# Kernel tuning notes

Hardware: AMD Instinct MI355X
Metric: run time of the kernel (lower is better)

## Reference

```python
import jax, jax.numpy as jnp
import numpy as np

B, S, E, H, L = 2, 2048, 1024, 16, 64


def setup_inputs() -> dict:
    key = jax.random.key(0)
    ks = jax.random.split(key, 9)
    x = jax.random.normal(ks[0], (B, S, E), dtype=jnp.float32)
    # causal mask: 1 where attention allowed, 0 where blocked (mask==0 -> -inf)
    mask = jnp.tril(jnp.ones((1, S, S), dtype=jnp.int32))
    std = 0.02
    # per-head Linear weights stacked over heads; torch Linear stores W as [out, in]
    Wq = jax.random.normal(ks[1], (H, L, E), dtype=jnp.float32) * std
    Wk = jax.random.normal(ks[2], (H, L, E), dtype=jnp.float32) * std
    Wv = jax.random.normal(ks[3], (H, L, E), dtype=jnp.float32) * std
    bq = jax.random.normal(ks[4], (H, L), dtype=jnp.float32) * std
    bk = jax.random.normal(ks[5], (H, L), dtype=jnp.float32) * std
    bv = jax.random.normal(ks[6], (H, L), dtype=jnp.float32) * std
    Wo = jax.random.normal(ks[7], (E, H * L), dtype=jnp.float32) * std
    bo = jax.random.normal(ks[8], (E,), dtype=jnp.float32) * std
    return {"x": x, "mask": mask, "Wq": Wq, "bq": bq, "Wk": Wk, "bk": bk,
            "Wv": Wv, "bv": bv, "Wo": Wo, "bo": bo}


def reference(x, mask, Wq, bq, Wk, bk, Wv, bv, Wo, bo):
    # Q/K/V for all heads at once: [B, H, S, L]
    Q = jnp.einsum('bse,hle->bhsl', x, Wq) + bq[None, :, None, :]
    K = jnp.einsum('bse,hle->bhsl', x, Wk) + bk[None, :, None, :]
    V = jnp.einsum('bse,hle->bhsl', x, Wv) + bv[None, :, None, :]
    scale = jnp.sqrt(jnp.asarray(L, dtype=Q.dtype))
    scores = jnp.einsum('bhsl,bhtl->bhst', Q, K) / scale  # [B,H,S,S]
    scores = jnp.where(mask[:, None, :, :] == 0, -jnp.inf, scores)
    P = jax.nn.softmax(scores, axis=-1)
    O = jnp.einsum('bhst,bhtl->bhsl', P, V)  # [B,H,S,L]
    # concat heads along last dim (head order matches torch concat)
    z = jnp.transpose(O, (0, 2, 1, 3)).reshape(O.shape[0], O.shape[2], -1)
    return jnp.einsum('bsk,ek->bse', z, Wo) + bo
```

## Files before the change

kernel.cpp:

```cpp
#include <hip/hip_runtime.h>
#include <math.h>

typedef unsigned short US;
typedef __attribute__((ext_vector_type(8))) __bf16 bf16x8;
typedef __attribute__((ext_vector_type(4))) float f32x4;
typedef __attribute__((ext_vector_type(4))) unsigned short us4;

#define MFMA16(a, b, c) __builtin_amdgcn_mfma_f32_16x16x32_bf16(a, b, c, 0, 0, 0)

__device__ __forceinline__ US f2bf(float f) {
  union { float f; unsigned u; } v; v.f = f;
  unsigned r = v.u + 0x7fffu + ((v.u >> 16) & 1u);
  return (US)(r >> 16);
}
__device__ __forceinline__ float bf2f(US u) {
  union { unsigned u; float f; } v; v.u = ((unsigned)u) << 16; return v.f;
}

__device__ __forceinline__ void gload16(const void* g, void* l) {
  __builtin_amdgcn_global_load_lds(
      (const __attribute__((address_space(1))) unsigned int*)g,
      (__attribute__((address_space(3))) unsigned int*)l, 16, 0, 0);
}

__global__ __launch_bounds__(256) void convert_k(
    const float* __restrict__ x, const float* __restrict__ Wq,
    const float* __restrict__ Wk, const float* __restrict__ Wv,
    const float* __restrict__ Wo,
    US* __restrict__ xb, US* __restrict__ wqkv, US* __restrict__ wob) {
  long i = (long)blockIdx.x * blockDim.x + threadIdx.x;
  long e4 = i * 4;
  if (e4 >= 8388608L) return;
  const float* src; US* dst;
  if (e4 < 4194304L) { src = x + e4; dst = xb + e4; }
  else if (e4 < 7340032L) {
    long off = e4 - 4194304L;
    dst = wqkv + off;
    src = (off < 1048576L) ? Wq + off
        : (off < 2097152L ? Wk + (off - 1048576L) : Wv + (off - 2097152L));
  } else {
    long off = e4 - 7340032L;
    src = Wo + off; dst = wob + off;
  }
  float4 v = *(const float4*)src;
  us4 o; o.x = f2bf(v.x); o.y = f2bf(v.y); o.z = f2bf(v.z); o.w = f2bf(v.w);
  *(us4*)dst = o;
}

template <int MODE>
__global__ __launch_bounds__(256) void gemm128(
    const US* __restrict__ A, const US* __restrict__ BT,
    int K, int lda, int ldb, int N,
    const float* __restrict__ b0, const float* __restrict__ b1,
    const float* __restrict__ b2,
    US* __restrict__ oQ, US* __restrict__ oK, US* __restrict__ oV,
    float* __restrict__ oF) {
  __shared__ __align__(16) US As[2][128 * 32];
  __shared__ __align__(16) US Bs[2][128 * 32];
  const int tid = threadIdx.x, lane = tid & 63;
  const int w = tid >> 6, wr = w >> 1, wc = w & 1;
  const int m0 = blockIdx.x * 128, n0 = blockIdx.y * 128;
  f32x4 acc[4][4] = {};
  const int r0 = tid >> 2, c0 = (tid & 3) * 8;

  for (int kt = 0; kt < K; kt += 64) {
#pragma unroll
    for (int h = 0; h < 2; ++h) {
      gload16(A + (size_t)(m0 + r0) * lda + kt + h * 32 + c0, As[h] + tid * 8);
      gload16(A + (size_t)(m0 + r0 + 64) * lda + kt + h * 32 + c0,
              As[h] + (tid + 256) * 8);
      gload16(BT + (size_t)(n0 + r0) * ldb + kt + h * 32 + c0, Bs[h] + tid * 8);
      gload16(BT + (size_t)(n0 + r0 + 64) * ldb + kt + h * 32 + c0,
              Bs[h] + (tid + 256) * 8);
    }
    __syncthreads();
#pragma unroll
    for (int h = 0; h < 2; ++h) {
      bf16x8 af[4], bfm[4];
#pragma unroll
      for (int i = 0; i < 4; ++i)
        af[i] = *(const bf16x8*)(As[h] + (wr * 64 + i * 16 + (lane & 15)) * 32 +
                                 (lane >> 4) * 8);
#pragma unroll
      for (int j = 0; j < 4; ++j)
        bfm[j] = *(const bf16x8*)(Bs[h] + (wc * 64 + j * 16 + (lane & 15)) * 32 +
                                  (lane >> 4) * 8);
#pragma unroll
      for (int i = 0; i < 4; ++i)
#pragma unroll
        for (int j = 0; j < 4; ++j)
          acc[i][j] = MFMA16(af[i], bfm[j], acc[i][j]);
    }
    __syncthreads();
  }

#pragma unroll
  for (int i = 0; i < 4; ++i) {
#pragma unroll
    for (int j = 0; j < 4; ++j) {
#pragma unroll
      for (int r = 0; r < 4; ++r) {
        int m = m0 + wr * 64 + i * 16 + (lane >> 4) * 4 + r;
        int n = n0 + wc * 64 + j * 16 + (lane & 15);
        float v = acc[i][j][r];
        if (MODE == 0) {
          int bb = m >> 11, s = m & 2047;
          int sec = n >> 10, idx = n & 1023;
          int h = idx >> 6, l = idx & 63;
          size_t bhsl = (((size_t)bb * 16 + h) * 2048 + s) * 64 + l;
          if (sec == 0)      oQ[bhsl] = f2bf((v + b0[idx]) * 0.18033688f);
          else if (sec == 1) oK[bhsl] = f2bf(v + b1[idx]);
          else oV[(((size_t)bb * 16 + h) * 64 + l) * 2048 + s] = f2bf(v + b2[idx]);
        } else {
          oF[(size_t)m * N + n] = v + b0[n];
        }
      }
    }
  }
}

__global__ __launch_bounds__(256) void attn_k(
    const US* __restrict__ Qb, const US* __restrict__ Kb,
    const US* __restrict__ Vtb, US* __restrict__ opart,
    float2* __restrict__ mlpart) {
  __shared__ __align__(16) US Ks[64 * 64];
  __shared__ __align__(16) US Vs[64 * 64];
  __shared__ __align__(16) US Ps[4][16 * 72];
  const int tid = threadIdx.x, lane = tid & 63, w = tid >> 6;
  const int slot = blockIdx.x >> 6;
  const int qt = 31 - slot;
  const int bh = (blockIdx.x & 63) >> 1;
  const int half = blockIdx.x & 1;
  const int h0 = (qt + 2) >> 1;
  const int kstart = half ? h0 : 0;
  const int kend = half ? (qt + 1) : h0;
  const size_t pslot = (size_t)(bh * 32 + qt) * 2 + half;

  if (kstart >= kend) {
    US* op = opart + pslot * 4096;
    us4 z; z.x = 0; z.y = 0; z.z = 0; z.w = 0;
#pragma unroll
    for (int j = 0; j < 4; ++j) *(us4*)(op + tid * 16 + j * 4) = z;
    if ((lane >> 4) == 0)
      mlpart[pslot * 64 + w * 16 + lane] = make_float2(-INFINITY, 0.f);
    return;
  }

  const US* Qp = Qb + ((size_t)bh * 2048 + qt * 64) * 64;
  const char* Kbase = (const char*)(Kb + (size_t)bh * 2048 * 64);
  const char* Vbase = (const char*)(Vtb + (size_t)bh * 64 * 2048);

  const int row0 = tid >> 3, col16 = (tid & 7) * 16;
  const int row1 = row0 + 32;
  const int soff0 = (row0 * 128 + col16) ^ ((row0 & 7) << 4);
  const int soff1 = soff0 + 32 * 128;

  bf16x8 aq[2];
  {
    int qrow = w * 16 + (lane & 15);
#pragma unroll
    for (int kk = 0; kk < 2; ++kk)
      aq[kk] = *(const bf16x8*)(Qp + qrow * 64 + kk * 32 + (lane >> 4) * 8);
  }
  f32x4 o[4] = {};
  float m = -INFINITY, l = 0.f;

  int4 rk0, rk1, rv0, rv1;
#define LOADT(KT)                                                              \
  do {                                                                         \
    rk0 = *(const int4*)(Kbase + ((size_t)((KT)*64 + row0)) * 128 + col16);    \
    rk1 = *(const int4*)(Kbase + ((size_t)((KT)*64 + row1)) * 128 + col16);    \
    rv0 = *(const int4*)(Vbase + (size_t)row0 * 4096 + (KT)*128 + col16);      \
    rv1 = *(const int4*)(Vbase + (size_t)row1 * 4096 + (KT)*128 + col16);      \
  } while (0)
#define WRITET()                                                               \
  do {                                                                         \
    *(int4*)((char*)Ks + soff0) = rk0;                                         \
    *(int4*)((char*)Ks + soff1) = rk1;                                         \
    *(int4*)((char*)Vs + soff0) = rv0;                                         \
    *(int4*)((char*)Vs + soff1) = rv1;                                         \
  } while (0)

  LOADT(kstart);
  WRITET();
  __syncthreads();

  for (int kt = kstart; kt < kend; ++kt) {
    if (kt + 1 < kend) LOADT(kt + 1);

    f32x4 sc[4];
    __builtin_amdgcn_s_setprio(1);
#pragma unroll
    for (int nt = 0; nt < 4; ++nt) {
      f32x4 s = {0.f, 0.f, 0.f, 0.f};
#pragma unroll
      for (int kk = 0; kk < 2; ++kk) {
        int rr = nt * 16 + (lane & 15);
        int off = rr * 128 + kk * 64 + (lane >> 4) * 16;
        off ^= (rr & 7) << 4;
        bf16x8 bkf = *(const bf16x8*)((const char*)Ks + off);
        s = MFMA16(bkf, aq[kk], s);
      }
      sc[nt] = s;
    }
    __builtin_amdgcn_s_setprio(0);

    if (kt == qt) {
      int q_in = w * 16 + (lane & 15);
#pragma unroll
      for (int nt = 0; nt < 4; ++nt)
#pragma unroll
        for (int r = 0; r < 4; ++r) {
          int kv_in = nt * 16 + (lane >> 4) * 4 + r;
          if (kv_in > q_in) sc[nt][r] = -INFINITY;
        }
    }

    {
      float m01 = fmaxf(fmaxf(sc[0][0], sc[0][1]), fmaxf(sc[0][2], sc[0][3]));
      float m23 = fmaxf(fmaxf(sc[1][0], sc[1][1]), fmaxf(sc[1][2], sc[1][3]));
      float m45 = fmaxf(fmaxf(sc[2][0], sc[2][1]), fmaxf(sc[2][2], sc[2][3]));
      float m67 = fmaxf(fmaxf(sc[3][0], sc[3][1]), fmaxf(sc[3][2], sc[3][3]));
      float mx = fmaxf(fmaxf(m01, m23), fmaxf(m45, m67));
      mx = fmaxf(mx, __shfl_xor(mx, 16));
      mx = fmaxf(mx, __shfl_xor(mx, 32));
      float mnew = fmaxf(m, mx);
      float scale = exp2f(m - mnew);
      m = mnew;
      float s0 = 0.f, s1 = 0.f, s2 = 0.f, s3 = 0.f;
#pragma unroll
      for (int nt = 0; nt < 4; ++nt) {
        float p0 = exp2f(sc[nt][0] - m);
        float p1 = exp2f(sc[nt][1] - m);
        float p2 = exp2f(sc[nt][2] - m);
        float p3 = exp2f(sc[nt][3] - m);
        sc[nt][0] = p0; sc[nt][1] = p1; sc[nt][2] = p2; sc[nt][3] = p3;
        s0 += p0; s1 += p1; s2 += p2; s3 += p3;
      }
      float ssum = (s0 + s1) + (s2 + s3);
      ssum += __shfl_xor(ssum, 16);
      ssum += __shfl_xor(ssum, 32);
      l = l * scale + ssum;
#pragma unroll
      for (int r = 0; r < 4; ++r) {
        float sr = __shfl(scale, ((lane >> 4) << 2) + r, 64);
        o[0][r] *= sr; o[1][r] *= sr; o[2][r] *= sr; o[3][r] *= sr;
      }
    }

    US* pp = &Ps[w][0];
    const int pbase = (lane & 15) * 72 + (lane >> 4) * 4;
#pragma unroll
    for (int nt = 0; nt < 4; ++nt) {
      us4 w4;
      w4.x = f2bf(sc[nt][0]); w4.y = f2bf(sc[nt][1]);
      w4.z = f2bf(sc[nt][2]); w4.w = f2bf(sc[nt][3]);
      *(us4*)(pp + pbase + nt * 16) = w4;
    }

    __builtin_amdgcn_s_setprio(1);
#pragma unroll
    for (int kk = 0; kk < 2; ++kk) {
      bf16x8 pa = *(const bf16x8*)(pp + (lane & 15) * 72 + kk * 32 + (lane >> 4) * 8);
#pragma unroll
      for (int nt = 0; nt < 4; ++nt) {
        int rr = nt * 16 + (lane & 15);
        int off = rr * 128 + kk * 64 + (lane >> 4) * 16;
        off ^= (rr & 7) << 4;
        bf16x8 bvf = *(const bf16x8*)((const char*)Vs + off);
        o[nt] = MFMA16(pa, bvf, o[nt]);
      }
    }
    __builtin_amdgcn_s_setprio(0);

    __syncthreads();
    if (kt + 1 < kend) {
      WRITET();
      __syncthreads();
    }
  }
#undef LOADT
#undef WRITET

  US* op = opart + pslot * 4096;
#pragma unroll
  for (int r = 0; r < 4; ++r) {
    int row = w * 16 + (lane >> 4) * 4 + r;
#pragma unroll
    for (int nt = 0; nt < 4; ++nt) {
      int d = nt * 16 + (lane & 15);
      op[row * 64 + d] = f2bf(o[nt][r]);
    }
  }
  if ((lane >> 4) == 0)
    mlpart[pslot * 64 + w * 16 + lane] = make_float2(m, l);
}

__global__ __launch_bounds__(256) void merge_k(
    const US* __restrict__ opart, const float2* __restrict__ mlpart,
    US* __restrict__ zb) {
  const int t = blockIdx.x;
  const int bh = t >> 5, qt = t & 31;
  const int b = bh >> 4, h = bh & 15;
  const int row = threadIdx.x >> 2;
  const int dg = (threadIdx.x & 3) * 16;
  const US* o1 = opart + ((size_t)t * 2 + 0) * 4096 + row * 64 + dg;
  const US* o2 = opart + ((size_t)t * 2 + 1) * 4096 + row * 64 + dg;
  float2 ml1 = mlpart[(t * 2 + 0) * 64 + row];
  float2 ml2 = mlpart[(t * 2 + 1) * 64 + row];
  float mm = fmaxf(ml1.x, ml2.x);
  float w1 = exp2f(ml1.x - mm), w2 = exp2f(ml2.x - mm);
  float li = 1.0f / (ml1.y * w1 + ml2.y * w2);
  w1 *= li; w2 *= li;
  int s = qt * 64 + row;
  US* dst = zb + ((size_t)b * 2048 + s) * 1024 + h * 64 + dg;
#pragma unroll
  for (int j = 0; j < 4; ++j) {
    us4 a = *(const us4*)(o1 + j * 4);
    us4 c = *(const us4*)(o2 + j * 4);
    us4 r;
    r.x = f2bf(bf2f(a.x) * w1 + bf2f(c.x) * w2);
    r.y = f2bf(bf2f(a.y) * w1 + bf2f(c.y) * w2);
    r.z = f2bf(bf2f(a.z) * w1 + bf2f(c.z) * w2);
    r.w = f2bf(bf2f(a.w) * w1 + bf2f(c.w) * w2);
    *(us4*)(dst + j * 4) = r;
  }
}

extern "C" void kernel_launch(void* const* d_in, const int* in_sizes, int n_in,
                              void* d_out, int out_size, void* d_ws, size_t ws_size,
                              hipStream_t stream) {
  (void)in_sizes; (void)n_in; (void)out_size; (void)ws_size;
  const float* x  = (const float*)d_in[0];
  const float* Wq = (const float*)d_in[2];
  const float* bq = (const float*)d_in[3];
  const float* Wk = (const float*)d_in[4];
  const float* bk = (const float*)d_in[5];
  const float* Wv = (const float*)d_in[6];
  const float* bv = (const float*)d_in[7];
  const float* Wo = (const float*)d_in[8];
  const float* bo = (const float*)d_in[9];
  char* ws = (char*)d_ws;
  US* xb     = (US*)(ws);
  float2* ml = (float2*)(ws);
  US* zb     = (US*)(ws + 1048576);
  US* wqkv   = (US*)(ws + 8388608);
  US* wob    = (US*)(ws + 14680064);
  US* Qb     = (US*)(ws + 16777216);
  US* Kb     = (US*)(ws + 25165824);
  US* Vtb    = (US*)(ws + 33554432);
  US* opart  = (US*)d_out;
  float* out = (float*)d_out;

  convert_k<<<dim3(8192), dim3(256), 0, stream>>>(x, Wq, Wk, Wv, Wo, xb, wqkv, wob);
  gemm128<0><<<dim3(32, 24), dim3(256), 0, stream>>>(
      xb, wqkv, 1024, 1024, 1024, 3072, bq, bk, bv, Qb, Kb, Vtb, (float*)nullptr);
  attn_k<<<dim3(2048), dim3(256), 0, stream>>>(Qb, Kb, Vtb, opart, ml);
  merge_k<<<dim3(1024), dim3(256), 0, stream>>>(opart, ml, zb);
  gemm128<1><<<dim3(32, 8), dim3(256), 0, stream>>>(
      zb, wob, 1024, 1024, 1024, 1024, bo, (const float*)nullptr, (const float*)nullptr,
      (US*)nullptr, (US*)nullptr, (US*)nullptr, out);
}
```

Measured before the change: 134.3 us.

## Replace QKV projection GEMM with 256x256 tiled, triple-buffered, 8-wave pipelined kernel

The QKV projection GEMM moves from 128x128 tiles with double buffering to 256x256 tiles on 512 threads. A three-stage LDS ring issues global-to-LDS loads two k-steps ahead, A and B staging are interleaved between two MFMA halves, and s_setprio raises priority around the MFMA blocks. The aim is more data reuse per tile and better overlap of memory loads with matrix math. In exchange there are only 192 blocks on a large GPU (under one wave of CUs), 96KB of LDS per block and higher register pressure. The output projection becomes a separate non-templated kernel with unchanged behaviour.

```diff
diff --git a/kernel.cpp b/kernel.cpp
--- a/kernel.cpp
+++ b/kernel.cpp
@@ -47,14 +47,113 @@
   *(us4*)dst = o;
 }
 
-template <int MODE>
-__global__ __launch_bounds__(256) void gemm128(
+__global__ __launch_bounds__(512, 2) void gemm256(
+    const US* __restrict__ A, const US* __restrict__ BT,
+    int K, int lda, int ldb,
+    const float* __restrict__ b0, const float* __restrict__ b1,
+    const float* __restrict__ b2,
+    US* __restrict__ oQ, US* __restrict__ oK, US* __restrict__ oV) {
+  __shared__ __align__(16) US As[3][256 * 32];
+  __shared__ __align__(16) US Bs[3][256 * 32];
+  const int tid = threadIdx.x, lane = tid & 63, wid = tid >> 6;
+  const int wr = wid >> 2, wc = wid & 3;
+  const int m0 = blockIdx.x * 256, n0 = blockIdx.y * 256;
+  f32x4 acc[8][4] = {};
+  const int srow = tid >> 2, scol = (tid & 3) * 8;
+  const int NT = K / 32;
+
+#define STAGE_A(BUF, T)                                                        \
+  do {                                                                         \
+    gload16(A + (size_t)(m0 + srow) * lda + (T) * 32 + scol,                   \
+            As[BUF] + tid * 8);                                                \
+    gload16(A + (size_t)(m0 + 128 + srow) * lda + (T) * 32 + scol,             \
+            As[BUF] + 4096 + tid * 8);                                         \
+  } while (0)
+#define STAGE_B(BUF, T)                                                        \
+  do {                                                                         \
+    gload16(BT + (size_t)(n0 + srow) * ldb + (T) * 32 + scol,                  \
+            Bs[BUF] + tid * 8);                                                \
+    gload16(BT + (size_t)(n0 + 128 + srow) * ldb + (T) * 32 + scol,            \
+            Bs[BUF] + 4096 + tid * 8);                                         \
+  } while (0)
+
+  STAGE_A(0, 0); STAGE_B(0, 0);
+  STAGE_A(1, 1); STAGE_B(1, 1);
+  asm volatile("s_waitcnt vmcnt(4)" ::: "memory");
+  __builtin_amdgcn_s_barrier();
+
+  for (int t = 0; t < NT; ++t) {
+    const int buf = t % 3;
+    const US* Ab = As[buf];
+    const US* Bb = Bs[buf];
+    bf16x8 bfr[4], afr[4];
+#pragma unroll
+    for (int j = 0; j < 4; ++j)
+      bfr[j] = *(const bf16x8*)(Bb + (wc * 64 + j * 16 + (lane & 15)) * 32 +
+                                (lane >> 4) * 8);
+#pragma unroll
+    for (int i = 0; i < 4; ++i)
+      afr[i] = *(const bf16x8*)(Ab + (wr * 128 + i * 16 + (lane & 15)) * 32 +
+                                (lane >> 4) * 8);
+    if (t + 2 < NT) STAGE_A((t + 2) % 3, t + 2);
+    __builtin_amdgcn_s_barrier();
+    asm volatile("s_waitcnt lgkmcnt(0)" ::: "memory");
+    __builtin_amdgcn_s_setprio(1);
+#pragma unroll
+    for (int i = 0; i < 4; ++i)
+#pragma unroll
+      for (int j = 0; j < 4; ++j)
+        acc[i][j] = MFMA16(afr[i], bfr[j], acc[i][j]);
+    __builtin_amdgcn_s_setprio(0);
+    __builtin_amdgcn_s_barrier();
+#pragma unroll
+    for (int i = 0; i < 4; ++i)
+      afr[i] = *(const bf16x8*)(Ab + (wr * 128 + (i + 4) * 16 + (lane & 15)) * 32 +
+                                (lane >> 4) * 8);
+    if (t + 2 < NT) STAGE_B((t + 2) % 3, t + 2);
+    __builtin_amdgcn_s_barrier();
+    asm volatile("s_waitcnt lgkmcnt(0)" ::: "memory");
+    __builtin_amdgcn_s_setprio(1);
+#pragma unroll
+    for (int i = 0; i < 4; ++i)
+#pragma unroll
+      for (int j = 0; j < 4; ++j)
+        acc[i + 4][j] = MFMA16(afr[i], bfr[j], acc[i + 4][j]);
+    __builtin_amdgcn_s_setprio(0);
+    if (t + 2 < NT)
+      asm volatile("s_waitcnt vmcnt(4)" ::: "memory");
+    else if (t + 1 < NT)
+      asm volatile("s_waitcnt vmcnt(0)" ::: "memory");
+    __builtin_amdgcn_s_barrier();
+  }
+#undef STAGE_A
+#undef STAGE_B
+
+#pragma unroll
+  for (int i = 0; i < 8; ++i) {
+#pragma unroll
+    for (int j = 0; j < 4; ++j) {
+#pragma unroll
+      for (int r = 0; r < 4; ++r) {
+        int m = m0 + wr * 128 + i * 16 + (lane >> 4) * 4 + r;
+        int n = n0 + wc * 64 + j * 16 + (lane & 15);
+        float v = acc[i][j][r];
+        int bb = m >> 11, s = m & 2047;
+        int sec = n >> 10, idx = n & 1023;
+        int h = idx >> 6, l = idx & 63;
+        size_t bhsl = (((size_t)bb * 16 + h) * 2048 + s) * 64 + l;
+        if (sec == 0)      oQ[bhsl] = f2bf((v + b0[idx]) * 0.18033688f);
+        else if (sec == 1) oK[bhsl] = f2bf(v + b1[idx]);
+        else oV[(((size_t)bb * 16 + h) * 64 + l) * 2048 + s] = f2bf(v + b2[idx]);
+      }
+    }
+  }
+}
+
+__global__ __launch_bounds__(256) void gemm128o(
     const US* __restrict__ A, const US* __restrict__ BT,
     int K, int lda, int ldb, int N,
-    const float* __restrict__ b0, const float* __restrict__ b1,
-    const float* __restrict__ b2,
-    US* __restrict__ oQ, US* __restrict__ oK, US* __restrict__ oV,
-    float* __restrict__ oF) {
+    const float* __restrict__ b0, float* __restrict__ oF) {
   __shared__ __align__(16) US As[2][128 * 32];
   __shared__ __align__(16) US Bs[2][128 * 32];
   const int tid = threadIdx.x, lane = tid & 63;
@@ -95,28 +194,15 @@
   }
 
 #pragma unroll
-  for (int i = 0; i < 4; ++i) {
-#pragma unroll
-    for (int j = 0; j < 4; ++j) {
+  for (int i = 0; i < 4; ++i)
+#pragma unroll
+    for (int j = 0; j < 4; ++j)
 #pragma unroll
       for (int r = 0; r < 4; ++r) {
         int m = m0 + wr * 64 + i * 16 + (lane >> 4) * 4 + r;
         int n = n0 + wc * 64 + j * 16 + (lane & 15);
-        float v = acc[i][j][r];
-        if (MODE == 0) {
-          int bb = m >> 11, s = m & 2047;
-          int sec = n >> 10, idx = n & 1023;
-          int h = idx >> 6, l = idx & 63;
-          size_t bhsl = (((size_t)bb * 16 + h) * 2048 + s) * 64 + l;
-          if (sec == 0)      oQ[bhsl] = f2bf((v + b0[idx]) * 0.18033688f);
-          else if (sec == 1) oK[bhsl] = f2bf(v + b1[idx]);
-          else oV[(((size_t)bb * 16 + h) * 64 + l) * 2048 + s] = f2bf(v + b2[idx]);
-        } else {
-          oF[(size_t)m * N + n] = v + b0[n];
-        }
-      }
-    }
-  }
+        oF[(size_t)m * N + n] = acc[i][j][r] + b0[n];
+      }
 }
 
 __global__ __launch_bounds__(256) void attn_k(
@@ -353,11 +439,10 @@
   float* out = (float*)d_out;
 
   convert_k<<<dim3(8192), dim3(256), 0, stream>>>(x, Wq, Wk, Wv, Wo, xb, wqkv, wob);
-  gemm128<0><<<dim3(32, 24), dim3(256), 0, stream>>>(
-      xb, wqkv, 1024, 1024, 1024, 3072, bq, bk, bv, Qb, Kb, Vtb, (float*)nullptr);
+  gemm256<<<dim3(16, 12), dim3(512), 0, stream>>>(
+      xb, wqkv, 1024, 1024, 1024, bq, bk, bv, Qb, Kb, Vtb);
   attn_k<<<dim3(2048), dim3(256), 0, stream>>>(Qb, Kb, Vtb, opart, ml);
   merge_k<<<dim3(1024), dim3(256), 0, stream>>>(opart, ml, zb);
-  gemm128<1><<<dim3(32, 8), dim3(256), 0, stream>>>(
-      zb, wob, 1024, 1024, 1024, 1024, bo, (const float*)nullptr, (const float*)nullptr,
-      (US*)nullptr, (US*)nullptr, (US*)nullptr, out);
-}
+  gemm128o<<<dim3(32, 8), dim3(256), 0, stream>>>(
+      zb, wob, 1024, 1024, 1024, 1024, bo, out);
+}
```

New measurement: 163.3 us. 1.22x slower.
